# Kernel tuning notes

Measured on AMD Instinct MI355X. Metric: run time of the kernel, lower is better.

Reference implementation:

```python
import jax, jax.numpy as jnp
import numpy as np

IN_DIM, HID_DIM, OUT_DIM, N_EXP = 1024, 4096, 1024, 8
BATCH = 8192


def setup_inputs() -> dict:
    key = jax.random.key(0)
    ks = jax.random.split(key, 8)
    s_in = 1.0 / np.sqrt(IN_DIM)
    s_hid = 1.0 / np.sqrt(HID_DIM)
    return {
        "x": jax.random.normal(ks[0], (BATCH, IN_DIM), jnp.float32),
        "router_w": jax.random.uniform(ks[1], (IN_DIM, N_EXP), jnp.float32, -s_in, s_in),
        "router_b": jax.random.uniform(ks[2], (N_EXP,), jnp.float32, -s_in, s_in),
        "expert_w": jax.random.uniform(ks[3], (N_EXP, IN_DIM, HID_DIM), jnp.float32, -s_in, s_in),
        "expert_b": jax.random.uniform(ks[4], (N_EXP, HID_DIM), jnp.float32, -s_in, s_in),
        "proj_w": jax.random.uniform(ks[5], (HID_DIM, OUT_DIM), jnp.float32, -s_hid, s_hid),
        "proj_b": jax.random.uniform(ks[6], (OUT_DIM,), jnp.float32, -s_hid, s_hid),
    }


def reference(x, router_w, router_b, expert_w, expert_b, proj_w, proj_b):
    # Hard routing: argmax over router logits selects one expert per token.
    logits = x @ router_w + router_b                 # [N, E]
    idx = jnp.argmax(logits, axis=-1)                # [N] int
    n_exp = expert_w.shape[0]
    # Masked per-expert GEMMs (loop over small fixed expert count), summed.
    h = jnp.zeros((x.shape[0], expert_w.shape[2]), dtype=x.dtype)
    for e in range(n_exp):
        mask = (idx == e)[:, None]                   # [N, 1]
        h = h + jnp.where(mask, x @ expert_w[e] + expert_b[e], 0.0)
    out = h @ proj_w + proj_b                        # [N, out_dim]
    routing_weights = jax.nn.one_hot(idx, n_exp, dtype=jnp.float32)
    return out, routing_weights
```

## Files before the change

kernel.cpp:

```cpp
#include <hip/hip_runtime.h>
#include <stdint.h>

#define B_TOK 8192
#define DIN 1024
#define DHID 4096
#define DOUT 1024
#define NE 8

typedef __bf16 bf16x8 __attribute__((ext_vector_type(8)));
typedef float f32x4 __attribute__((ext_vector_type(4)));

__device__ __forceinline__ unsigned short f2bf(float f) {
  union { float f; unsigned u; } v; v.f = f;
  unsigned r = v.u + 0x7fffu + ((v.u >> 16) & 1u);
  return (unsigned short)(r >> 16);
}

__device__ __forceinline__ void async16(const void* g, void* l) {
  __builtin_amdgcn_global_load_lds(
      (__attribute__((address_space(1))) void*)const_cast<void*>(g),
      (__attribute__((address_space(3))) void*)l, 16, 0, 0);
}

__global__ __launch_bounds__(256) void router_kernel(
    const float* __restrict__ x, const float* __restrict__ rw,
    const float* __restrict__ rb, float* __restrict__ oh,
    unsigned short* __restrict__ xb, int* __restrict__ idx,
    int* __restrict__ pos, int* __restrict__ counts)
{
  const int token = blockIdx.x * 4 + (threadIdx.x >> 6);
  const int lane = threadIdx.x & 63;
  const float* xrow = x + (size_t)token * DIN;
  double acc[NE];
#pragma unroll
  for (int e = 0; e < NE; ++e) acc[e] = 0.0;

#pragma unroll
  for (int j = 0; j < 4; ++j) {
    const int v4 = j * 64 + lane;
    const float4 xv = ((const float4*)xrow)[v4];
    const float4* rwr = (const float4*)(rw + (size_t)v4 * 32);
#pragma unroll
    for (int c = 0; c < 4; ++c) {
      const float xs = (&xv.x)[c];
      const float4 w0 = rwr[c * 2 + 0];
      const float4 w1 = rwr[c * 2 + 1];
      acc[0] += (double)(xs * w0.x); acc[1] += (double)(xs * w0.y);
      acc[2] += (double)(xs * w0.z); acc[3] += (double)(xs * w0.w);
      acc[4] += (double)(xs * w1.x); acc[5] += (double)(xs * w1.y);
      acc[6] += (double)(xs * w1.z); acc[7] += (double)(xs * w1.w);
    }
    ushort4 us;
    us.x = f2bf(xv.x); us.y = f2bf(xv.y); us.z = f2bf(xv.z); us.w = f2bf(xv.w);
    ((ushort4*)(xb + (size_t)token * DIN))[v4] = us;
  }
#pragma unroll
  for (int off = 32; off > 0; off >>= 1)
#pragma unroll
    for (int e = 0; e < NE; ++e) acc[e] += __shfl_xor(acc[e], off, 64);

  if (lane == 0) {
    double best = -1e300; int be = 0;
#pragma unroll
    for (int e = 0; e < NE; ++e) {
      const double v = acc[e] + (double)rb[e];
      if (v > best) { best = v; be = e; }
    }
    idx[token] = be;
    pos[token] = atomicAdd(&counts[be], 1);
    float* o = oh + (size_t)token * NE;
#pragma unroll
    for (int e = 0; e < NE; ++e) o[e] = (e == be) ? 1.f : 0.f;
  }
}

__global__ __launch_bounds__(256) void transpose_bf16(
    const float* __restrict__ in, unsigned short* __restrict__ out, int K, int N)
{
  __shared__ float tile[64][65];
  const size_t mat = (size_t)blockIdx.z * (size_t)K * N;
  const int k0 = blockIdx.x * 64, n0 = blockIdx.y * 64;
  const int c = threadIdx.x & 63, r0 = threadIdx.x >> 6;
#pragma unroll
  for (int rr = 0; rr < 64; rr += 4)
    tile[rr + r0][c] = in[mat + (size_t)(k0 + rr + r0) * N + n0 + c];
  __syncthreads();
#pragma unroll
  for (int rr = 0; rr < 64; rr += 4) {
    const int n2 = rr + r0;
    out[mat + (size_t)(n0 + n2) * K + k0 + c] = f2bf(tile[c][n2]);
  }
}

__global__ void slots_kernel(const int* __restrict__ counts, int* __restrict__ offsets,
                             int* __restrict__ slot_e, int* __restrict__ slot_g0,
                             int* __restrict__ slot_nr, int* __restrict__ nslots)
{
  int off = 0, s = 0;
  offsets[0] = 0;
  for (int e = 0; e < NE; ++e) {
    const int c = counts[e];
    for (int t = 0; t < c; t += 256) {
      slot_e[s] = e; slot_g0[s] = off + t;
      slot_nr[s] = (c - t < 256) ? (c - t) : 256;
      ++s;
    }
    off += c;
    offsets[e + 1] = off;
  }
  *nslots = s;
}

__global__ __launch_bounds__(256) void scatter_kernel(
    const int* __restrict__ idx, const int* __restrict__ pos,
    const int* __restrict__ offsets, int* __restrict__ perm)
{
  const int t = blockIdx.x * 256 + threadIdx.x;
  perm[offsets[idx[t]] + pos[t]] = t;
}

__global__ __launch_bounds__(512) void expert_gemm(
    const unsigned short* __restrict__ xb, const unsigned short* __restrict__ Wt,
    const float* __restrict__ eb, const int* __restrict__ perm,
    const int* __restrict__ slot_e, const int* __restrict__ slot_g0,
    const int* __restrict__ slot_nr, const int* __restrict__ nslots,
    unsigned short* __restrict__ h)
{
  const int id = blockIdx.x;
  const int s = id >> 4;
  const int ntile = id & 15;
  if (s >= *nslots) return;
  const int e = slot_e[s];
  const int g0 = slot_g0[s];
  const int nr = slot_nr[s];
  const int n0 = ntile * 256;

  __shared__ __align__(16) unsigned short lsA[2][256 * 64];
  __shared__ __align__(16) unsigned short lsB[2][256 * 64];

  const int tid = threadIdx.x;
  const int w = tid >> 6, lane = tid & 63;
  const int rgrp = lane >> 3, cch = lane & 7;
  const int sw8 = (cch ^ rgrp) * 8;
  const int wr = w >> 2, wc = w & 3;
  const int quad = lane >> 4, l15 = lane & 15;

  const unsigned short* ap[4];
#pragma unroll
  for (int sub = 0; sub < 4; ++sub) {
    const int row = sub * 64 + w * 8 + rgrp;
    ap[sub] = xb + (size_t)perm[g0 + (row < nr ? row : 0)] * DIN + sw8;
  }
  const unsigned short* wbp = Wt + (size_t)e * DHID * DIN;
  const unsigned short* bp[4];
#pragma unroll
  for (int sub = 0; sub < 4; ++sub)
    bp[sub] = wbp + (size_t)(n0 + sub * 64 + w * 8 + rgrp) * DIN + sw8;

  f32x4 acc[8][4];
  const f32x4 z = {0.f, 0.f, 0.f, 0.f};
#pragma unroll
  for (int i = 0; i < 8; ++i)
#pragma unroll
    for (int j = 0; j < 4; ++j) acc[i][j] = z;

  auto stageA = [&](int db, int k0) {
#pragma unroll
    for (int sub = 0; sub < 4; ++sub)
      async16(ap[sub] + k0, &lsA[db][(sub * 64 + w * 8) * 64]);
  };
  auto stageB = [&](int db, int k0) {
#pragma unroll
    for (int sub = 0; sub < 4; ++sub)
      async16(bp[sub] + k0, &lsB[db][(sub * 64 + w * 8) * 64]);
  };

  auto phase = [&](int db, int ks, bool dostage, int k0n) {
    bf16x8 af[8], bfv[4];
    const int q = ks * 4 + quad;
#pragma unroll
    for (int i = 0; i < 8; ++i) {
      const int row = wr * 128 + i * 16 + l15;
      af[i] = *(const bf16x8*)&lsA[db][row * 64 + ((q ^ (row & 7)) << 3)];
    }
#pragma unroll
    for (int j = 0; j < 4; ++j) {
      const int row = wc * 64 + j * 16 + l15;
      bfv[j] = *(const bf16x8*)&lsB[db][row * 64 + ((q ^ (row & 7)) << 3)];
    }
    if (dostage) stageB(db ^ 1, k0n);
    __builtin_amdgcn_s_barrier();
    asm volatile("s_waitcnt lgkmcnt(0)" ::: "memory");
    __builtin_amdgcn_sched_barrier(0);
    __builtin_amdgcn_s_setprio(1);
#pragma unroll
    for (int i = 0; i < 8; ++i)
#pragma unroll
      for (int j = 0; j < 4; ++j)
        acc[i][j] = __builtin_amdgcn_mfma_f32_16x16x32_bf16(af[i], bfv[j], acc[i][j], 0, 0, 0);
    __builtin_amdgcn_s_setprio(0);
    __builtin_amdgcn_s_barrier();
  };

  auto tile = [&](int db, int t, bool notlast) {
    if (notlast) {
      stageA(db ^ 1, (t + 1) * 64);
      asm volatile("s_waitcnt vmcnt(4)" ::: "memory");
    } else {
      asm volatile("s_waitcnt vmcnt(0)" ::: "memory");
    }
    __builtin_amdgcn_s_barrier();
    phase(db, 0, notlast, (t + 1) * 64);
    phase(db, 1, false, 0);
  };

  stageA(0, 0);
  stageB(0, 0);
  constexpr int NT = DIN / 64;
  for (int t = 0; t < NT; t += 2) {
    tile(0, t, true);
    tile(1, t + 1, t + 2 < NT);
  }

#pragma unroll
  for (int j = 0; j < 4; ++j) {
    const int col = n0 + wc * 64 + j * 16 + l15;
    const float bias = eb[e * DHID + col];
#pragma unroll
    for (int i = 0; i < 8; ++i)
#pragma unroll
      for (int r2 = 0; r2 < 4; ++r2) {
        const int row = wr * 128 + i * 16 + quad * 4 + r2;
        if (row < nr)
          h[(size_t)(g0 + row) * DHID + col] = f2bf(acc[i][j][r2] + bias);
      }
  }
}

__global__ __launch_bounds__(512) void proj_gemm(
    const unsigned short* __restrict__ hm, const unsigned short* __restrict__ Pt,
    const float* __restrict__ pb, const int* __restrict__ perm,
    float* __restrict__ out)
{
  const int id = blockIdx.x;
  const int m0 = (id & 31) * 256;
  const int n0 = (id >> 5) * 128;

  __shared__ __align__(16) unsigned short lsA[2][256 * 64];
  __shared__ __align__(16) unsigned short lsB[2][128 * 64];

  const int tid = threadIdx.x;
  const int w = tid >> 6, lane = tid & 63;
  const int rgrp = lane >> 3, cch = lane & 7;
  const int sw8 = (cch ^ rgrp) * 8;
  const int wr = w >> 2, wc = w & 3;
  const int quad = lane >> 4, l15 = lane & 15;

  const unsigned short* ap[4];
#pragma unroll
  for (int hh = 0; hh < 2; ++hh)
#pragma unroll
    for (int l = 0; l < 2; ++l) {
      const int row = m0 + hh * 128 + l * 64 + w * 8 + rgrp;
      ap[hh * 2 + l] = hm + (size_t)row * DHID + sw8;
    }
  const unsigned short* bp[2];
#pragma unroll
  for (int hh = 0; hh < 2; ++hh)
    bp[hh] = Pt + (size_t)(n0 + hh * 64 + w * 8 + rgrp) * DHID + sw8;

  f32x4 acc[8][2];
  const f32x4 z = {0.f, 0.f, 0.f, 0.f};
#pragma unroll
  for (int i = 0; i < 8; ++i) { acc[i][0] = z; acc[i][1] = z; }

  auto stageA0 = [&](int db, int k0) {
    async16(ap[0] + k0, &lsA[db][(w * 8) * 64]);
    async16(ap[1] + k0, &lsA[db][(64 + w * 8) * 64]);
  };
  auto stageRest = [&](int db, int k0) {
    async16(ap[2] + k0, &lsA[db][(128 + w * 8) * 64]);
    async16(ap[3] + k0, &lsA[db][(192 + w * 8) * 64]);
    async16(bp[0] + k0, &lsB[db][(w * 8) * 64]);
    async16(bp[1] + k0, &lsB[db][(64 + w * 8) * 64]);
  };

  auto phase = [&](int db, int ks, bool dostage, int k0n) {
    bf16x8 af[8], bfv[2];
    const int q = ks * 4 + quad;
#pragma unroll
    for (int i = 0; i < 8; ++i) {
      const int row = wr * 128 + i * 16 + l15;
      af[i] = *(const bf16x8*)&lsA[db][row * 64 + ((q ^ (row & 7)) << 3)];
    }
#pragma unroll
    for (int j = 0; j < 2; ++j) {
      const int row = wc * 32 + j * 16 + l15;
      bfv[j] = *(const bf16x8*)&lsB[db][row * 64 + ((q ^ (row & 7)) << 3)];
    }
    if (dostage) stageRest(db ^ 1, k0n);
    __builtin_amdgcn_s_barrier();
    asm volatile("s_waitcnt lgkmcnt(0)" ::: "memory");
    __builtin_amdgcn_sched_barrier(0);
    __builtin_amdgcn_s_setprio(1);
#pragma unroll
    for (int i = 0; i < 8; ++i)
#pragma unroll
      for (int j = 0; j < 2; ++j)
        acc[i][j] = __builtin_amdgcn_mfma_f32_16x16x32_bf16(af[i], bfv[j], acc[i][j], 0, 0, 0);
    __builtin_amdgcn_s_setprio(0);
    __builtin_amdgcn_s_barrier();
  };

  auto tile = [&](int db, int t, bool notlast) {
    if (notlast) {
      stageA0(db ^ 1, (t + 1) * 64);
      asm volatile("s_waitcnt vmcnt(2)" ::: "memory");
    } else {
      asm volatile("s_waitcnt vmcnt(0)" ::: "memory");
    }
    __builtin_amdgcn_s_barrier();
    phase(db, 0, notlast, (t + 1) * 64);
    phase(db, 1, false, 0);
  };

  stageA0(0, 0);
  stageRest(0, 0);
  constexpr int NT = DHID / 64;
  for (int t = 0; t < NT; t += 2) {
    tile(0, t, true);
    tile(1, t + 1, t + 2 < NT);
  }

#pragma unroll
  for (int i = 0; i < 8; ++i)
#pragma unroll
    for (int r2 = 0; r2 < 4; ++r2) {
      const int row = m0 + wr * 128 + i * 16 + quad * 4 + r2;
      const int orow = perm[row];
#pragma unroll
      for (int j = 0; j < 2; ++j) {
        const int col = n0 + wc * 32 + j * 16 + l15;
        out[(size_t)orow * DOUT + col] = acc[i][j][r2] + pb[col];
      }
    }
}

extern "C" void kernel_launch(void* const* d_in, const int* in_sizes, int n_in,
                              void* d_out, int out_size, void* d_ws, size_t ws_size,
                              hipStream_t stream)
{
  const float* x  = (const float*)d_in[0];
  const float* rw = (const float*)d_in[1];
  const float* rb = (const float*)d_in[2];
  const float* ew = (const float*)d_in[3];
  const float* eb = (const float*)d_in[4];
  const float* pw = (const float*)d_in[5];
  const float* pb = (const float*)d_in[6];
  float* out = (float*)d_out;
  float* oh  = out + (size_t)B_TOK * DOUT;

  char* ws = (char*)d_ws;
  constexpr size_t OXB = 0;
  constexpr size_t OWT = OXB + (size_t)B_TOK * DIN * 2;
  constexpr size_t OPT = OWT + (size_t)NE * DHID * DIN * 2;
  constexpr size_t OH  = OPT + (size_t)DOUT * DHID * 2;
  constexpr size_t OIDX = OH + (size_t)B_TOK * DHID * 2;
  constexpr size_t OPOS = OIDX + (size_t)B_TOK * 4;
  constexpr size_t OPRM = OPOS + (size_t)B_TOK * 4;
  constexpr size_t OCNT = OPRM + (size_t)B_TOK * 4;
  constexpr size_t OOFF = OCNT + 256;
  constexpr size_t OSE  = OOFF + 256;
  constexpr size_t OSG  = OSE + 512;
  constexpr size_t OSN  = OSG + 512;
  constexpr size_t ONS  = OSN + 512;
  constexpr size_t NEED = ONS + 512;

  if (ws_size < NEED) {
    hipMemsetAsync(d_out, 0, (size_t)out_size * 4, stream);
    return;
  }

  unsigned short* xb   = (unsigned short*)(ws + OXB);
  unsigned short* Wt   = (unsigned short*)(ws + OWT);
  unsigned short* Pt   = (unsigned short*)(ws + OPT);
  unsigned short* h    = (unsigned short*)(ws + OH);
  int* idx     = (int*)(ws + OIDX);
  int* pos     = (int*)(ws + OPOS);
  int* perm    = (int*)(ws + OPRM);
  int* counts  = (int*)(ws + OCNT);
  int* offsets = (int*)(ws + OOFF);
  int* slot_e  = (int*)(ws + OSE);
  int* slot_g0 = (int*)(ws + OSG);
  int* slot_nr = (int*)(ws + OSN);
  int* nslots  = (int*)(ws + ONS);

  hipMemsetAsync(counts, 0, 64, stream);
  router_kernel<<<B_TOK / 4, 256, 0, stream>>>(x, rw, rb, oh, xb, idx, pos, counts);
  transpose_bf16<<<dim3(DIN / 64, DHID / 64, NE), 256, 0, stream>>>(ew, Wt, DIN, DHID);
  transpose_bf16<<<dim3(DHID / 64, DOUT / 64, 1), 256, 0, stream>>>(pw, Pt, DHID, DOUT);
  slots_kernel<<<1, 1, 0, stream>>>(counts, offsets, slot_e, slot_g0, slot_nr, nslots);
  scatter_kernel<<<B_TOK / 256, 256, 0, stream>>>(idx, pos, offsets, perm);
  expert_gemm<<<40 * 16, 512, 0, stream>>>(
      xb, Wt, eb, perm, slot_e, slot_g0, slot_nr, nslots, h);
  proj_gemm<<<(DOUT / 128) * (B_TOK / 256), 512, 0, stream>>>(h, Pt, pb, perm, out);
}
```

Baseline: 585.3 us.

## Simplify GEMM main loops to plain double-buffered staging with full barriers

Both the expert GEMM and the projection GEMM drop their hand-scheduled two-phase pipeline. That pipeline used split A/B staging, explicit vmcnt/lgkmcnt waits and sched barriers. In its place is one loop per tile: issue all async loads for the next tile, compute both k-substeps from the current buffer, then __syncthreads. The epilogues also hoist the bias loads out of the row loops. The code is simpler and leaves scheduling to the compiler, but it may lose the finer-grained overlap of LDS reads, global loads and MFMA that the tuned version had, since each iteration now waits on all outstanding memory.

```diff
diff --git a/kernel.cpp b/kernel.cpp
--- a/kernel.cpp
+++ b/kernel.cpp
@@ -164,77 +164,64 @@
 #pragma unroll
     for (int j = 0; j < 4; ++j) acc[i][j] = z;
 
-  auto stageA = [&](int db, int k0) {
-#pragma unroll
-    for (int sub = 0; sub < 4; ++sub)
+  auto stage = [&](int db, int k0) {
+#pragma unroll
+    for (int sub = 0; sub < 4; ++sub) {
       async16(ap[sub] + k0, &lsA[db][(sub * 64 + w * 8) * 64]);
+      async16(bp[sub] + k0, &lsB[db][(sub * 64 + w * 8) * 64]);
+    }
   };
-  auto stageB = [&](int db, int k0) {
-#pragma unroll
-    for (int sub = 0; sub < 4; ++sub)
-      async16(bp[sub] + k0, &lsB[db][(sub * 64 + w * 8) * 64]);
-  };
-
-  auto phase = [&](int db, int ks, bool dostage, int k0n) {
-    bf16x8 af[8], bfv[4];
-    const int q = ks * 4 + quad;
-#pragma unroll
-    for (int i = 0; i < 8; ++i) {
-      const int row = wr * 128 + i * 16 + l15;
-      af[i] = *(const bf16x8*)&lsA[db][row * 64 + ((q ^ (row & 7)) << 3)];
-    }
-#pragma unroll
-    for (int j = 0; j < 4; ++j) {
-      const int row = wc * 64 + j * 16 + l15;
-      bfv[j] = *(const bf16x8*)&lsB[db][row * 64 + ((q ^ (row & 7)) << 3)];
-    }
-    if (dostage) stageB(db ^ 1, k0n);
-    __builtin_amdgcn_s_barrier();
-    asm volatile("s_waitcnt lgkmcnt(0)" ::: "memory");
-    __builtin_amdgcn_sched_barrier(0);
+
+  stage(0, 0);
+  __syncthreads();
+
+  constexpr int NT = DIN / 64;
+  for (int t = 0; t < NT; ++t) {
+    const int cur = t & 1;
+    if (t + 1 < NT) stage(cur ^ 1, (t + 1) * 64);
+
     __builtin_amdgcn_s_setprio(1);
 #pragma unroll
-    for (int i = 0; i < 8; ++i)
-#pragma unroll
-      for (int j = 0; j < 4; ++j)
-        acc[i][j] = __builtin_amdgcn_mfma_f32_16x16x32_bf16(af[i], bfv[j], acc[i][j], 0, 0, 0);
+    for (int ks = 0; ks < 2; ++ks) {
+      const int q = ks * 4 + quad;
+      bf16x8 af[8], bfv[4];
+#pragma unroll
+      for (int i = 0; i < 8; ++i) {
+        const int row = wr * 128 + i * 16 + l15;
+        af[i] = *(const bf16x8*)&lsA[cur][row * 64 + ((q ^ (row & 7)) << 3)];
+      }
+#pragma unroll
+      for (int j = 0; j < 4; ++j) {
+        const int row = wc * 64 + j * 16 + l15;
+        bfv[j] = *(const bf16x8*)&lsB[cur][row * 64 + ((q ^ (row & 7)) << 3)];
+      }
+#pragma unroll
+      for (int i = 0; i < 8; ++i)
+#pragma unroll
+        for (int j = 0; j < 4; ++j)
+          acc[i][j] = __builtin_amdgcn_mfma_f32_16x16x32_bf16(af[i], bfv[j], acc[i][j], 0, 0, 0);
+    }
     __builtin_amdgcn_s_setprio(0);
-    __builtin_amdgcn_s_barrier();
-  };
-
-  auto tile = [&](int db, int t, bool notlast) {
-    if (notlast) {
-      stageA(db ^ 1, (t + 1) * 64);
-      asm volatile("s_waitcnt vmcnt(4)" ::: "memory");
-    } else {
-      asm volatile("s_waitcnt vmcnt(0)" ::: "memory");
-    }
-    __builtin_amdgcn_s_barrier();
-    phase(db, 0, notlast, (t + 1) * 64);
-    phase(db, 1, false, 0);
-  };
-
-  stageA(0, 0);
-  stageB(0, 0);
-  constexpr int NT = DIN / 64;
-  for (int t = 0; t < NT; t += 2) {
-    tile(0, t, true);
-    tile(1, t + 1, t + 2 < NT);
-  }
-
-#pragma unroll
-  for (int j = 0; j < 4; ++j) {
-    const int col = n0 + wc * 64 + j * 16 + l15;
-    const float bias = eb[e * DHID + col];
-#pragma unroll
-    for (int i = 0; i < 8; ++i)
-#pragma unroll
-      for (int r2 = 0; r2 < 4; ++r2) {
-        const int row = wr * 128 + i * 16 + quad * 4 + r2;
-        if (row < nr)
-          h[(size_t)(g0 + row) * DHID + col] = f2bf(acc[i][j][r2] + bias);
-      }
-  }
+
+    __syncthreads();
+  }
+
+  float bias[4];
+#pragma unroll
+  for (int j = 0; j < 4; ++j)
+    bias[j] = eb[e * DHID + n0 + wc * 64 + j * 16 + l15];
+#pragma unroll
+  for (int i = 0; i < 8; ++i)
+#pragma unroll
+    for (int r2 = 0; r2 < 4; ++r2) {
+      const int row = wr * 128 + i * 16 + quad * 4 + r2;
+      if (row < nr) {
+        unsigned short* hr = h + (size_t)(g0 + row) * DHID + n0 + wc * 64;
+#pragma unroll
+        for (int j = 0; j < 4; ++j)
+          hr[j * 16 + l15] = f2bf(acc[i][j][r2] + bias[j]);
+      }
+    }
 }
 
 __global__ __launch_bounds__(512) void proj_gemm(
@@ -258,12 +245,10 @@
 
   const unsigned short* ap[4];
 #pragma unroll
-  for (int hh = 0; hh < 2; ++hh)
-#pragma unroll
-    for (int l = 0; l < 2; ++l) {
-      const int row = m0 + hh * 128 + l * 64 + w * 8 + rgrp;
-      ap[hh * 2 + l] = hm + (size_t)row * DHID + sw8;
-    }
+  for (int sub = 0; sub < 4; ++sub) {
+    const int row = m0 + sub * 64 + w * 8 + rgrp;
+    ap[sub] = hm + (size_t)row * DHID + sw8;
+  }
   const unsigned short* bp[2];
 #pragma unroll
   for (int hh = 0; hh < 2; ++hh)
@@ -274,75 +259,63 @@
 #pragma unroll
   for (int i = 0; i < 8; ++i) { acc[i][0] = z; acc[i][1] = z; }
 
-  auto stageA0 = [&](int db, int k0) {
-    async16(ap[0] + k0, &lsA[db][(w * 8) * 64]);
-    async16(ap[1] + k0, &lsA[db][(64 + w * 8) * 64]);
+  auto stage = [&](int db, int k0) {
+#pragma unroll
+    for (int sub = 0; sub < 4; ++sub)
+      async16(ap[sub] + k0, &lsA[db][(sub * 64 + w * 8) * 64]);
+#pragma unroll
+    for (int hh = 0; hh < 2; ++hh)
+      async16(bp[hh] + k0, &lsB[db][(hh * 64 + w * 8) * 64]);
   };
-  auto stageRest = [&](int db, int k0) {
-    async16(ap[2] + k0, &lsA[db][(128 + w * 8) * 64]);
-    async16(ap[3] + k0, &lsA[db][(192 + w * 8) * 64]);
-    async16(bp[0] + k0, &lsB[db][(w * 8) * 64]);
-    async16(bp[1] + k0, &lsB[db][(64 + w * 8) * 64]);
-  };
-
-  auto phase = [&](int db, int ks, bool dostage, int k0n) {
-    bf16x8 af[8], bfv[2];
-    const int q = ks * 4 + quad;
-#pragma unroll
-    for (int i = 0; i < 8; ++i) {
-      const int row = wr * 128 + i * 16 + l15;
-      af[i] = *(const bf16x8*)&lsA[db][row * 64 + ((q ^ (row & 7)) << 3)];
-    }
-#pragma unroll
-    for (int j = 0; j < 2; ++j) {
-      const int row = wc * 32 + j * 16 + l15;
-      bfv[j] = *(const bf16x8*)&lsB[db][row * 64 + ((q ^ (row & 7)) << 3)];
-    }
-    if (dostage) stageRest(db ^ 1, k0n);
-    __builtin_amdgcn_s_barrier();
-    asm volatile("s_waitcnt lgkmcnt(0)" ::: "memory");
-    __builtin_amdgcn_sched_barrier(0);
+
+  stage(0, 0);
+  __syncthreads();
+
+  constexpr int NT = DHID / 64;
+  for (int t = 0; t < NT; ++t) {
+    const int cur = t & 1;
+    if (t + 1 < NT) stage(cur ^ 1, (t + 1) * 64);
+
     __builtin_amdgcn_s_setprio(1);
 #pragma unroll
-    for (int i = 0; i < 8; ++i)
-#pragma unroll
-      for (int j = 0; j < 2; ++j)
-        acc[i][j] = __builtin_amdgcn_mfma_f32_16x16x32_bf16(af[i], bfv[j], acc[i][j], 0, 0, 0);
+    for (int ks = 0; ks < 2; ++ks) {
+      const int q = ks * 4 + quad;
+      bf16x8 af[8], bfv[2];
+#pragma unroll
+      for (int i = 0; i < 8; ++i) {
+        const int row = wr * 128 + i * 16 + l15;
+        af[i] = *(const bf16x8*)&lsA[cur][row * 64 + ((q ^ (row & 7)) << 3)];
+      }
+#pragma unroll
+      for (int j = 0; j < 2; ++j) {
+        const int row = wc * 32 + j * 16 + l15;
+        bfv[j] = *(const bf16x8*)&lsB[cur][row * 64 + ((q ^ (row & 7)) << 3)];
+      }
+#pragma unroll
+      for (int i = 0; i < 8; ++i)
+#pragma unroll
+        for (int j = 0; j < 2; ++j)
+          acc[i][j] = __builtin_amdgcn_mfma_f32_16x16x32_bf16(af[i], bfv[j], acc[i][j], 0, 0, 0);
+    }
     __builtin_amdgcn_s_setprio(0);
-    __builtin_amdgcn_s_barrier();
-  };
-
-  auto tile = [&](int db, int t, bool notlast) {
-    if (notlast) {
-      stageA0(db ^ 1, (t + 1) * 64);
-      asm volatile("s_waitcnt vmcnt(2)" ::: "memory");
-    } else {
-      asm volatile("s_waitcnt vmcnt(0)" ::: "memory");
-    }
-    __builtin_amdgcn_s_barrier();
-    phase(db, 0, notlast, (t + 1) * 64);
-    phase(db, 1, false, 0);
-  };
-
-  stageA0(0, 0);
-  stageRest(0, 0);
-  constexpr int NT = DHID / 64;
-  for (int t = 0; t < NT; t += 2) {
-    tile(0, t, true);
-    tile(1, t + 1, t + 2 < NT);
-  }
-
+
+    __syncthreads();
+  }
+
+  float pbj[2];
+#pragma unroll
+  for (int j = 0; j < 2; ++j)
+    pbj[j] = pb[n0 + wc * 32 + j * 16 + l15];
 #pragma unroll
   for (int i = 0; i < 8; ++i)
 #pragma unroll
     for (int r2 = 0; r2 < 4; ++r2) {
       const int row = m0 + wr * 128 + i * 16 + quad * 4 + r2;
       const int orow = perm[row];
-#pragma unroll
-      for (int j = 0; j < 2; ++j) {
-        const int col = n0 + wc * 32 + j * 16 + l15;
-        out[(size_t)orow * DOUT + col] = acc[i][j][r2] + pb[col];
-      }
+      float* orp = out + (size_t)orow * DOUT + n0 + wc * 32;
+#pragma unroll
+      for (int j = 0; j < 2; ++j)
+        orp[j * 16 + l15] = acc[i][j][r2] + pbj[j];
     }
 }
 
```

Result: faster. 564.8 us (-3.5%).
